# Kernel optimization log

Measured on AMD Instinct MI355X. Metric: run time of the kernel, lower is better.

The kernel has to match this reference:

```python
import jax, jax.numpy as jnp
import numpy as np
import math

S, H, NH, HD = 2048, 1280, 16, 80
WIN = 64
NW = S // WIN
I = 3420
OUT = 3584
L = 8
FULL_IDX = (3, 7)
MERGE = 4  # spatial_merge_size**2
EPS = 1e-6


def setup_inputs() -> dict:
    key = jax.random.key(0)
    ks = jax.random.split(key, 16)
    w = lambda k, s: jax.random.normal(k, s, jnp.float32) * 0.02
    # rotary tables: half-dim freqs duplicated, as in Qwen2.5-VL vision rotary
    inv_freq = 1.0 / (10000.0 ** (np.arange(0, HD // 2, dtype=np.float32) / (HD // 2)))
    freqs = np.outer(np.arange(S, dtype=np.float32), inv_freq)  # [S, HD/2]
    emb = np.concatenate([freqs, freqs], axis=-1)               # [S, HD]
    return {
        "hidden_states": jax.random.normal(ks[0], (S, H), jnp.float32),
        "full_attn_masks": jnp.ones((1, 1, S, S), jnp.float32),
        "window_attn_masks": jnp.ones((NW, 1, WIN, WIN), jnp.float32),
        "cos": jnp.asarray(np.cos(emb)),
        "sin": jnp.asarray(np.sin(emb)),
        "qkv_w": w(ks[1], (L, 3 * H, H)),
        "qkv_b": w(ks[2], (L, 3 * H)),
        "proj_w": w(ks[3], (L, H, H)),
        "proj_b": w(ks[4], (L, H)),
        "norm1_w": jnp.ones((L, H), jnp.float32),
        "norm2_w": jnp.ones((L, H), jnp.float32),
        "gate_w": w(ks[5], (L, I, H)),
        "gate_b": w(ks[6], (L, I)),
        "up_w": w(ks[7], (L, I, H)),
        "up_b": w(ks[8], (L, I)),
        "down_w": w(ks[9], (L, H, I)),
        "down_b": w(ks[10], (L, H)),
        "ln_q_w": jnp.ones((H,), jnp.float32),
        "m0_w": w(ks[11], (H * MERGE, H * MERGE)),
        "m0_b": w(ks[12], (H * MERGE,)),
        "m2_w": w(ks[13], (OUT, H * MERGE)),
        "m2_b": w(ks[14], (OUT,)),
    }


def rmsnorm(x, w):
    v = jnp.mean(jnp.square(x.astype(jnp.float32)), axis=-1, keepdims=True)
    return (x * jax.lax.rsqrt(v + EPS)) * w


def rotate_half(x):
    x1, x2 = jnp.split(x, 2, axis=-1)
    return jnp.concatenate([-x2, x1], axis=-1)


def apply_rope(q, k, cos, sin):
    return q * cos + rotate_half(q) * sin, k * cos + rotate_half(k) * sin


def attn_full(x, mask, cos, sin, qkv_w, qkv_b, proj_w, proj_b):
    # x: [S, H]; mask: [1, 1, S, S] (additive)
    qkv = (x @ qkv_w.T + qkv_b).reshape(S, 3, NH, HD)
    q, k, v = [t[:, i].transpose(1, 0, 2) for i, t in [(0, qkv), (1, qkv), (2, qkv)]]  # [NH, S, HD]
    q, k = apply_rope(q, k, cos, sin)  # cos/sin [S, HD] broadcast over heads
    aw = jnp.einsum('hsd,htd->hst', q, k) / math.sqrt(HD) + mask[0]
    aw = jax.nn.softmax(aw.astype(jnp.float32), axis=-1)
    o = jnp.einsum('hst,htd->hsd', aw, v).transpose(1, 0, 2).reshape(S, NH * HD)
    return o @ proj_w.T + proj_b


def attn_window(x, mask, cos, sin, qkv_w, qkv_b, proj_w, proj_b):
    xw = x.reshape(NW, WIN, H)
    qkv = (xw @ qkv_w.T + qkv_b).reshape(NW, WIN, 3, NH, HD).transpose(2, 0, 3, 1, 4)
    q, k, v = qkv[0], qkv[1], qkv[2]
    cw = cos.reshape(NW, 1, WIN, HD)
    sw = sin.reshape(NW, 1, WIN, HD)
    q, k = apply_rope(q, k, cw, sw)
    aw = jnp.einsum('whsd,whtd->whst', q, k) / math.sqrt(HD) + mask
    aw = jax.nn.softmax(aw.astype(jnp.float32), axis=-1)
    o = jnp.einsum('whst,whtd->whsd', aw, v).transpose(0, 2, 1, 3).reshape(S, NH * HD)
    return o @ proj_w.T + proj_b


def reference(hidden_states, full_attn_masks, window_attn_masks, cos, sin,
              qkv_w, qkv_b, proj_w, proj_b, norm1_w, norm2_w,
              gate_w, gate_b, up_w, up_b, down_w, down_b,
              ln_q_w, m0_w, m0_b, m2_w, m2_b):
    NEG = jnp.finfo(jnp.float32).min
    fm = (1.0 - full_attn_masks) * NEG
    wm = (1.0 - window_attn_masks) * NEG
    x = hidden_states
    for i in range(L):
        h = rmsnorm(x, norm1_w[i])
        if i in FULL_IDX:
            a = attn_full(h, fm, cos, sin, qkv_w[i], qkv_b[i], proj_w[i], proj_b[i])
        else:
            a = attn_window(h, wm, cos, sin, qkv_w[i], qkv_b[i], proj_w[i], proj_b[i])
        x = x + a
        h = rmsnorm(x, norm2_w[i])
        mlp = (jax.nn.silu(h @ gate_w[i].T + gate_b[i]) * (h @ up_w[i].T + up_b[i])) @ down_w[i].T + down_b[i]
        x = x + mlp
    # patch merger: RMSNorm -> merge 4 tokens -> Linear-GELU-Linear
    h = rmsnorm(x, ln_q_w).reshape(-1, H * MERGE)  # [S/4, 5120]
    h = jax.nn.gelu(h @ m0_w.T + m0_b, approximate=False)
    return h @ m2_w.T + m2_b  # [S/4, OUT]
```

## Files before the change

### kernel.cpp

```cpp
#include <hip/hip_runtime.h>
#include <hip/hip_bf16.h>
#include <math.h>

#define S_LEN 2048
#define HID   1280
#define NHEADS 16
#define HDIM  80
#define HDP   96
#define VROWS 96
#define LAYERS 8
#define IDIM  3420
#define IDIMP 3456
#define MERGED 5120
#define OUTD  3584
#define NCH   4
#define CHLEN 512

typedef __attribute__((ext_vector_type(8))) short short8;
typedef __attribute__((ext_vector_type(4))) float f32x4;
typedef __attribute__((ext_vector_type(16))) float f32x16;
typedef unsigned int u32;
typedef __attribute__((ext_vector_type(4))) u32 u32x4;
typedef __attribute__((address_space(1))) const u32* gptr_t;
typedef __attribute__((address_space(3))) u32* lptr_t;

__device__ inline unsigned short f2b(float f){
  __hip_bfloat16 b = __float2bfloat16(f);
  return __builtin_bit_cast(unsigned short, b);
}
__device__ inline float b2f(unsigned short u){
  return __bfloat162float(__builtin_bit_cast(__hip_bfloat16, u));
}
__device__ inline unsigned pk2(float lo, float hi){
  return (unsigned)f2b(lo) | ((unsigned)f2b(hi) << 16);
}

__global__ __launch_bounds__(256) void convert_kernel(
    const float* __restrict__ src, unsigned short* __restrict__ dst,
    int N, int K, int Np, int Kp)
{
  int kg = Kp >> 3;
  size_t total = (size_t)Np * kg;
  for (size_t i = (size_t)blockIdx.x * 256 + threadIdx.x; i < total;
       i += (size_t)gridDim.x * 256){
    int k8 = (int)(i % kg);
    int n  = (int)(i / kg);
    int k0 = k8 * 8;
    u32 out[4];
    if (n < N && k0 + 8 <= K){
      const float* s = src + (size_t)n * K + k0;
      float4 f0 = *(const float4*)s;
      float4 f1 = *(const float4*)(s + 4);
      out[0] = pk2(f0.x, f0.y); out[1] = pk2(f0.z, f0.w);
      out[2] = pk2(f1.x, f1.y); out[3] = pk2(f1.z, f1.w);
    } else {
      #pragma unroll
      for (int j = 0; j < 4; ++j){
        int ka = k0 + 2 * j;
        float lo = (n < N && ka     < K) ? src[(size_t)n * K + ka]     : 0.f;
        float hi = (n < N && ka + 1 < K) ? src[(size_t)n * K + ka + 1] : 0.f;
        out[j] = pk2(lo, hi);
      }
    }
    *(uint4*)(dst + i * 8) = make_uint4(out[0], out[1], out[2], out[3]);
  }
}

__global__ __launch_bounds__(256) void concat_bias_kernel(
    const float* __restrict__ g, const float* __restrict__ u, float* __restrict__ o)
{
  int n = blockIdx.x * 256 + threadIdx.x;
  if (n >= 2 * IDIMP) return;
  if (n < IDIMP) o[n] = (n < IDIM) ? g[n] : 0.f;
  else { int m2 = n - IDIMP; o[n] = (m2 < IDIM) ? u[m2] : 0.f; }
}

__global__ __launch_bounds__(256) void rmsnorm_kernel(
    const float* __restrict__ x, const float* __restrict__ w,
    unsigned short* __restrict__ out, int H)
{
  int s = blockIdx.x;
  const float* row = x + (size_t)s * H;
  float ss = 0.f;
  for (int c = threadIdx.x; c < H; c += 256){ float v = row[c]; ss += v * v; }
  #pragma unroll
  for (int off = 32; off >= 1; off >>= 1) ss += __shfl_xor(ss, off, 64);
  __shared__ float red[4];
  if ((threadIdx.x & 63) == 0) red[threadIdx.x >> 6] = ss;
  __syncthreads();
  ss = red[0] + red[1] + red[2] + red[3];
  float rs = rsqrtf(ss / H + 1e-6f);
  unsigned short* orow = out + (size_t)s * H;
  for (int c = threadIdx.x; c < H; c += 256) orow[c] = f2b(row[c] * rs * w[c]);
}

template<int EPI, int BM>
__global__ __launch_bounds__(256) void gemm_kernel(
    const unsigned short* __restrict__ A, int lda,
    const unsigned short* __restrict__ B, int ldb,
    const float* __restrict__ bias, int Nact,
    void* __restrict__ Cv, int ldc,
    const float* __restrict__ res,
    int K)
{
  constexpr int MI = BM / 32;
  __shared__ __align__(16) unsigned short As[2][BM * 32];
  __shared__ __align__(16) unsigned short Bs[2][4096];
  const int tid  = threadIdx.x;
  const int lane = tid & 63;
  const int wave = tid >> 6;
  const int wm = wave >> 1, wn = wave & 1;
  const int m0 = blockIdx.y * BM, n0 = blockIdx.x * 128;
  const int l16 = lane & 15, lh = lane >> 4;
  const int lrow = lane >> 2;
  const int lcol = lane & 3;
  f32x4 acc[MI][4] = {};

  auto stage = [&](int bufi, int k0){
    #pragma unroll
    for (int j = 0; j < BM / 64; ++j){
      int chunk = wave * (BM / 64) + j;
      int row  = chunk * 16 + lrow;
      int slot = lcol ^ ((row >> 1) & 3);
      const unsigned short* srcA = A + (size_t)(m0 + row) * lda + k0 + slot * 8;
      __builtin_amdgcn_global_load_lds((gptr_t)srcA, (lptr_t)&As[bufi][chunk * 512], 16, 0, 0);
    }
    #pragma unroll
    for (int j = 0; j < 2; ++j){
      int chunk = wave * 2 + j;
      int row  = chunk * 16 + lrow;
      int slot = lcol ^ ((row >> 1) & 3);
      const unsigned short* srcB = B + (size_t)(n0 + row) * ldb + k0 + slot * 8;
      __builtin_amdgcn_global_load_lds((gptr_t)srcB, (lptr_t)&Bs[bufi][chunk * 512], 16, 0, 0);
    }
  };

  const int nt = K >> 5;
  stage(0, 0);
  __syncthreads();
  int buf = 0;
  for (int t = 0; t < nt; ++t){
    if (t + 1 < nt) stage(buf ^ 1, (t + 1) << 5);
    short8 af[MI], bfr[4];
    #pragma unroll
    for (int mi = 0; mi < MI; ++mi){
      int r = wm * (BM / 2) + mi * 16 + l16;
      int sl = lh ^ ((r >> 1) & 3);
      af[mi] = *(const short8*)&As[buf][r * 32 + sl * 8];
    }
    #pragma unroll
    for (int ni = 0; ni < 4; ++ni){
      int r = wn * 64 + ni * 16 + l16;
      int sl = lh ^ ((r >> 1) & 3);
      bfr[ni] = *(const short8*)&Bs[buf][r * 32 + sl * 8];
    }
    #pragma unroll
    for (int mi = 0; mi < MI; ++mi)
      #pragma unroll
      for (int ni = 0; ni < 4; ++ni)
        acc[mi][ni] = __builtin_amdgcn_mfma_f32_16x16x32_bf16(af[mi], bfr[ni], acc[mi][ni], 0, 0, 0);
    __syncthreads();
    buf ^= 1;
  }

  #pragma unroll
  for (int mi = 0; mi < MI; ++mi){
    int row = m0 + wm * (BM / 2) + mi * 16 + lh * 4;
    #pragma unroll
    for (int ni = 0; ni < 4; ++ni){
      int gn = n0 + wn * 64 + ni * 16 + l16;
      float bv = (gn < Nact) ? bias[gn] : 0.f;
      #pragma unroll
      for (int r2 = 0; r2 < 4; ++r2){
        float v = acc[mi][ni][r2] + bv;
        size_t offc = (size_t)(row + r2) * ldc + gn;
        if (EPI == 0)      ((float*)Cv)[offc] = v;
        else if (EPI == 1) ((float*)Cv)[offc] = res[offc] + v;
        else if (EPI == 2) ((unsigned short*)Cv)[offc] = f2b(0.5f * v * (1.0f + erff(v * 0.70710678118f)));
        else               ((unsigned short*)Cv)[offc] = f2b(v);
      }
    }
  }
}

__global__ __launch_bounds__(256) void rope_split_kernel(
    const unsigned short* __restrict__ qkv, const float* __restrict__ cosT,
    const float* __restrict__ sinT,
    unsigned short* __restrict__ qo, unsigned short* __restrict__ ko,
    unsigned short* __restrict__ vt)
{
  int s = blockIdx.x;
  const unsigned short* row = qkv + (size_t)s * 3840;
  #pragma unroll
  for (int it = 0; it < 5; ++it){
    int idx = it * 256 + threadIdx.x;
    int h = idx / 80, d = idx % 80;
    float qv = b2f(row[h * 80 + d]);
    float kv = b2f(row[1280 + h * 80 + d]);
    float vv = b2f(row[2560 + h * 80 + d]);
    float c  = cosT[s * 80 + d], sn = sinT[s * 80 + d];
    float qr = (d < 40) ? -b2f(row[h * 80 + d + 40])        : b2f(row[h * 80 + d - 40]);
    float kr = (d < 40) ? -b2f(row[1280 + h * 80 + d + 40]) : b2f(row[1280 + h * 80 + d - 40]);
    size_t qkoff = ((size_t)h * S_LEN + s) * HDP + d;
    qo[qkoff] = f2b(qv * c + qr * sn);
    ko[qkoff] = f2b(kv * c + kr * sn);
    vt[((size_t)h * VROWS + d) * S_LEN + s] = f2b(vv);
  }
  int h2 = threadIdx.x >> 4, d2 = 80 + (threadIdx.x & 15);
  size_t poff = ((size_t)h2 * S_LEN + s) * HDP + d2;
  qo[poff] = 0; ko[poff] = 0;
}

template<int PART>
__global__ __launch_bounds__(256) void flash_kernel(
    const unsigned short* __restrict__ q, const unsigned short* __restrict__ k,
    const unsigned short* __restrict__ vt, unsigned short* __restrict__ out,
    float* __restrict__ opart, float* __restrict__ mlpart)
{
  __shared__ unsigned short ot[4][32][88];
  const int lane = threadIdx.x & 63;
  const int w = threadIdx.x >> 6;
  const int h = blockIdx.y;
  const int l31 = lane & 31, lh1 = lane >> 5;
  const int qr = blockIdx.x * 128 + w * 32;
  const int ch = PART ? blockIdx.z : 0;
  const unsigned short* qh = q + (size_t)h * S_LEN * HDP;
  const unsigned short* kh = k + (size_t)h * S_LEN * HDP;
  const unsigned short* vh = vt + (size_t)h * VROWS * S_LEN;

  short8 qa[5];
  #pragma unroll
  for (int kc = 0; kc < 5; ++kc)
    qa[kc] = *(const short8*)(qh + (size_t)(qr + l31) * HDP + kc * 16 + lh1 * 8);

  float m_ = -1e30f, l_ = 0.f;
  f32x16 o0 = {}, o1 = {}, o2 = {};
  const int kvb = PART ? ch * CHLEN : (qr & ~63);
  const int kve = PART ? ch * CHLEN + CHLEN : (qr & ~63) + 64;
  const float scale = 0.11180339887498949f;

  for (int kvt = kvb; kvt < kve; kvt += 32){
    f32x16 sc = {};
    __builtin_amdgcn_s_setprio(1);
    #pragma unroll
    for (int kc = 0; kc < 5; ++kc){
      short8 kf = *(const short8*)(kh + (size_t)(kvt + l31) * HDP + kc * 16 + lh1 * 8);
      sc = __builtin_amdgcn_mfma_f32_32x32x16_bf16(kf, qa[kc], sc, 0, 0, 0);
    }
    __builtin_amdgcn_s_setprio(0);
    float t = sc[0];
    #pragma unroll
    for (int i = 1; i < 16; ++i) t = fmaxf(t, sc[i]);
    t = fmaxf(t, __shfl_xor(t, 32)) * scale;
    if (!__all(t <= m_ + 8.f)){
      float mnew = fmaxf(m_, t);
      float corr = __expf(m_ - mnew);
      l_ *= corr;
      #pragma unroll
      for (int i = 0; i < 16; ++i){ o0[i] *= corr; o1[i] *= corr; o2[i] *= corr; }
      m_ = mnew;
    }
    float p[16];
    float rs = 0.f;
    #pragma unroll
    for (int i = 0; i < 16; ++i){ p[i] = __expf(sc[i] * scale - m_); rs += p[i]; }
    rs += __shfl_xor(rs, 32);
    l_ += rs;
    unsigned wd0[4], wd1[4];
    #pragma unroll
    for (int j = 0; j < 2; ++j){
      unsigned Aj = pk2(p[2 * j],     p[2 * j + 1]);
      unsigned Bj = pk2(p[4 + 2 * j], p[4 + 2 * j + 1]);
      unsigned t0 = __shfl_xor(Aj, 32);
      unsigned t1 = __shfl_xor(Bj, 32);
      wd0[j]     = lh1 ? t1 : Aj;
      wd0[2 + j] = lh1 ? Bj : t0;
      Aj = pk2(p[8 + 2 * j],  p[8 + 2 * j + 1]);
      Bj = pk2(p[12 + 2 * j], p[12 + 2 * j + 1]);
      t0 = __shfl_xor(Aj, 32);
      t1 = __shfl_xor(Bj, 32);
      wd1[j]     = lh1 ? t1 : Aj;
      wd1[2 + j] = lh1 ? Bj : t0;
    }
    __builtin_amdgcn_s_setprio(1);
    #pragma unroll
    for (int kc2 = 0; kc2 < 2; ++kc2){
      u32x4 uw = kc2 ? u32x4{wd1[0], wd1[1], wd1[2], wd1[3]}
                     : u32x4{wd0[0], wd0[1], wd0[2], wd0[3]};
      short8 pb = __builtin_bit_cast(short8, uw);
      const unsigned short* vb = vh + kvt + kc2 * 16 + lh1 * 8;
      o0 = __builtin_amdgcn_mfma_f32_32x32x16_bf16(
          *(const short8*)(vb + (size_t)(l31)      * S_LEN), pb, o0, 0, 0, 0);
      o1 = __builtin_amdgcn_mfma_f32_32x32x16_bf16(
          *(const short8*)(vb + (size_t)(32 + l31) * S_LEN), pb, o1, 0, 0, 0);
      o2 = __builtin_amdgcn_mfma_f32_32x32x16_bf16(
          *(const short8*)(vb + (size_t)(64 + l31) * S_LEN), pb, o2, 0, 0, 0);
    }
    __builtin_amdgcn_s_setprio(0);
  }

  if (PART){
    const size_t hb = (size_t)(ch * NHEADS + h) * 80;
    #pragma unroll
    for (int r = 0; r < 16; ++r){
      int dl = (r & 3) + 8 * (r >> 2) + 4 * lh1;
      opart[(hb + dl)      * S_LEN + qr + l31] = o0[r];
      opart[(hb + 32 + dl) * S_LEN + qr + l31] = o1[r];
      if (dl < 16) opart[(hb + 64 + dl) * S_LEN + qr + l31] = o2[r];
    }
    if (lane < 32){
      size_t mb = ((size_t)(ch * NHEADS + h) * S_LEN + qr + l31) * 2;
      mlpart[mb] = m_; mlpart[mb + 1] = l_;
    }
  } else {
    float inv = 1.f / l_;
    #pragma unroll
    for (int r = 0; r < 16; ++r){
      int dl = (r & 3) + 8 * (r >> 2) + 4 * lh1;
      ot[w][l31][dl]      = f2b(o0[r] * inv);
      ot[w][l31][32 + dl] = f2b(o1[r] * inv);
      if (dl < 16) ot[w][l31][64 + dl] = f2b(o2[r] * inv);
    }
    int qq = lane >> 1, half = lane & 1;
    #pragma unroll
    for (int j = 0; j < 20; ++j){
      unsigned v = *(const unsigned*)&ot[w][qq][half * 40 + j * 2];
      *(unsigned*)&out[(size_t)(qr + qq) * HID + h * HDIM + half * 40 + j * 2] = v;
    }
  }
}

__global__ __launch_bounds__(256) void flash_reduce_kernel(
    const float* __restrict__ opart, const float* __restrict__ mlpart,
    unsigned short* __restrict__ out)
{
  __shared__ float wn[NCH][256];
  __shared__ unsigned short ot[256][82];
  const int tid = threadIdx.x;
  const int h = blockIdx.y;
  const int q0 = blockIdx.x * 256;
  float mv[NCH], lv[NCH];
  float M = -1e30f;
  #pragma unroll
  for (int c = 0; c < NCH; ++c){
    size_t mb = ((size_t)(c * NHEADS + h) * S_LEN + q0 + tid) * 2;
    mv[c] = mlpart[mb]; lv[c] = mlpart[mb + 1];
    M = fmaxf(M, mv[c]);
  }
  float L = 0.f;
  #pragma unroll
  for (int c = 0; c < NCH; ++c){ mv[c] = __expf(mv[c] - M); L += mv[c] * lv[c]; }
  float invL = 1.f / L;
  #pragma unroll
  for (int c = 0; c < NCH; ++c) wn[c][tid] = mv[c] * invL;
  __syncthreads();
  for (int d = 0; d < HDIM; ++d){
    float acc = 0.f;
    #pragma unroll
    for (int c = 0; c < NCH; ++c)
      acc += wn[c][tid] * opart[((size_t)(c * NHEADS + h) * 80 + d) * S_LEN + q0 + tid];
    ot[tid][d] = f2b(acc);
  }
  __syncthreads();
  #pragma unroll
  for (int j = 0; j < 40; ++j){
    unsigned v = *(const unsigned*)&ot[tid][j * 2];
    *(unsigned*)&out[(size_t)(q0 + tid) * HID + h * HDIM + j * 2] = v;
  }
}

__global__ __launch_bounds__(256) void silu_mul_kernel(
    const float* __restrict__ gu, unsigned short* __restrict__ out)
{
  size_t i = ((size_t)blockIdx.x * 256 + threadIdx.x) * 4;
  if (i >= (size_t)S_LEN * IDIMP) return;
  int row = (int)(i / IDIMP), col = (int)(i % IDIMP);
  float4 gv = *(const float4*)(gu + (size_t)row * (2 * IDIMP) + col);
  float4 uv = *(const float4*)(gu + (size_t)row * (2 * IDIMP) + IDIMP + col);
  float r0 = gv.x / (1.f + __expf(-gv.x)) * uv.x;
  float r1 = gv.y / (1.f + __expf(-gv.y)) * uv.y;
  float r2 = gv.z / (1.f + __expf(-gv.z)) * uv.z;
  float r3 = gv.w / (1.f + __expf(-gv.w)) * uv.w;
  uint2 o;
  o.x = pk2(r0, r1); o.y = pk2(r2, r3);
  *(uint2*)(out + i) = o;
}

static inline int cgrid(size_t total){
  size_t b = (total + 255) / 256;
  return (int)(b < 4096 ? b : 4096);
}

extern "C" void kernel_launch(void* const* d_in, const int* in_sizes, int n_in,
                              void* d_out, int out_size, void* d_ws, size_t ws_size,
                              hipStream_t stream)
{
  const float* hidden = (const float*)d_in[0];
  const float* cosT   = (const float*)d_in[3];
  const float* sinT   = (const float*)d_in[4];
  const float* qkv_w  = (const float*)d_in[5];
  const float* qkv_b  = (const float*)d_in[6];
  const float* proj_w = (const float*)d_in[7];
  const float* proj_b = (const float*)d_in[8];
  const float* norm1_w= (const float*)d_in[9];
  const float* norm2_w= (const float*)d_in[10];
  const float* gate_w = (const float*)d_in[11];
  const float* gate_b = (const float*)d_in[12];
  const float* up_w   = (const float*)d_in[13];
  const float* up_b   = (const float*)d_in[14];
  const float* down_w = (const float*)d_in[15];
  const float* down_b = (const float*)d_in[16];
  const float* ln_q_w = (const float*)d_in[17];
  const float* m0_w   = (const float*)d_in[18];
  const float* m0_b   = (const float*)d_in[19];
  const float* m2_w   = (const float*)d_in[20];
  const float* m2_b   = (const float*)d_in[21];

  char* ws = (char*)d_ws;
  size_t off = 0;
  auto carve = [&](size_t bytes)->char*{
    char* p = ws + off; off += (bytes + 255) & ~(size_t)255; return p;
  };
  float*          x    = (float*)         carve((size_t)S_LEN * HID * 4);
  unsigned short* hbuf = (unsigned short*)carve((size_t)S_LEN * HID * 2);
  unsigned short* qkvb = (unsigned short*)carve((size_t)S_LEN * 3840 * 2);
  unsigned short* qp   = (unsigned short*)carve((size_t)NHEADS * S_LEN * HDP * 2);
  unsigned short* kp   = (unsigned short*)carve((size_t)NHEADS * S_LEN * HDP * 2);
  unsigned short* vtb  = (unsigned short*)carve((size_t)NHEADS * VROWS * S_LEN * 2);
  unsigned short* ao   = (unsigned short*)carve((size_t)S_LEN * HID * 2);
  float*          gbuf = (float*)         carve((size_t)S_LEN * 2 * IDIMP * 4);
  unsigned short* mlp  = (unsigned short*)carve((size_t)S_LEN * IDIMP * 2);
  unsigned short* mg   = (unsigned short*)carve((size_t)512 * MERGED * 2);
  float*          opart= (float*)         carve((size_t)NCH * NHEADS * 80 * S_LEN * 4);
  float*          mlpt = (float*)         carve((size_t)NCH * NHEADS * S_LEN * 2 * 4);
  float*          cbias= (float*)         carve((size_t)2 * IDIMP * 4);
  unsigned short* wbig = (unsigned short*)carve((size_t)45000000 * 2);
  unsigned short* wqkv = wbig;
  unsigned short* wproj= wbig +  4915200;
  unsigned short* wgate= wproj + 1638400;
  unsigned short* wup  = wgate + (size_t)IDIMP * HID;
  unsigned short* wdown= wup   + (size_t)IDIMP * HID;
  unsigned short* wm0  = wbig;
  unsigned short* wm2  = wbig + (size_t)MERGED * MERGED;
  (void)ws_size; (void)in_sizes; (void)n_in; (void)out_size;

  hipMemcpyAsync(x, hidden, (size_t)S_LEN * HID * 4, hipMemcpyDeviceToDevice, stream);

  for (int i = 0; i < LAYERS; ++i){
    convert_kernel<<<cgrid((size_t)3840*HID/8), 256, 0, stream>>>(
        qkv_w + (size_t)i*3840*HID, wqkv, 3840, HID, 3840, HID);
    convert_kernel<<<cgrid((size_t)HID*HID/8), 256, 0, stream>>>(
        proj_w + (size_t)i*HID*HID, wproj, HID, HID, HID, HID);
    convert_kernel<<<cgrid((size_t)IDIMP*HID/8), 256, 0, stream>>>(
        gate_w + (size_t)i*IDIM*HID, wgate, IDIM, HID, IDIMP, HID);
    convert_kernel<<<cgrid((size_t)IDIMP*HID/8), 256, 0, stream>>>(
        up_w + (size_t)i*IDIM*HID, wup, IDIM, HID, IDIMP, HID);
    convert_kernel<<<cgrid((size_t)HID*IDIMP/8), 256, 0, stream>>>(
        down_w + (size_t)i*HID*IDIM, wdown, HID, IDIM, HID, IDIMP);
    concat_bias_kernel<<<27, 256, 0, stream>>>(
        gate_b + (size_t)i*IDIM, up_b + (size_t)i*IDIM, cbias);

    rmsnorm_kernel<<<S_LEN, 256, 0, stream>>>(x, norm1_w + (size_t)i * HID, hbuf, HID);
    gemm_kernel<3,128><<<dim3(30, 16), 256, 0, stream>>>(
        hbuf, HID, wqkv, HID, qkv_b + (size_t)i * 3840, 3840,
        qkvb, 3840, nullptr, HID);
    rope_split_kernel<<<S_LEN, 256, 0, stream>>>(qkvb, cosT, sinT, qp, kp, vtb);
    if (i == 3 || i == 7){
      flash_kernel<1><<<dim3(16, 16, NCH), 256, 0, stream>>>(qp, kp, vtb, nullptr, opart, mlpt);
      flash_reduce_kernel<<<dim3(8, 16), 256, 0, stream>>>(opart, mlpt, ao);
    } else {
      flash_kernel<0><<<dim3(16, 16), 256, 0, stream>>>(qp, kp, vtb, ao, nullptr, nullptr);
    }
    gemm_kernel<1,64><<<dim3(10, 32), 256, 0, stream>>>(
        ao, HID, wproj, HID, proj_b + (size_t)i * HID, HID,
        x, HID, x, HID);
    rmsnorm_kernel<<<S_LEN, 256, 0, stream>>>(x, norm2_w + (size_t)i * HID, hbuf, HID);
    gemm_kernel<0,128><<<dim3(54, 16), 256, 0, stream>>>(
        hbuf, HID, wgate, HID, cbias, 2 * IDIMP,
        gbuf, 2 * IDIMP, nullptr, HID);
    silu_mul_kernel<<<(int)(((size_t)S_LEN * IDIMP / 4 + 255) / 256), 256, 0, stream>>>(gbuf, mlp);
    gemm_kernel<1,64><<<dim3(10, 32), 256, 0, stream>>>(
        mlp, IDIMP, wdown, IDIMP, down_b + (size_t)i * HID, HID,
        x, HID, x, IDIMP);
  }
  convert_kernel<<<cgrid((size_t)MERGED*MERGED/8), 256, 0, stream>>>(
      m0_w, wm0, MERGED, MERGED, MERGED, MERGED);
  convert_kernel<<<cgrid((size_t)OUTD*MERGED/8), 256, 0, stream>>>(
      m2_w, wm2, OUTD, MERGED, OUTD, MERGED);
  rmsnorm_kernel<<<S_LEN, 256, 0, stream>>>(x, ln_q_w, hbuf, HID);
  gemm_kernel<2,64><<<dim3(40, 8), 256, 0, stream>>>(
      hbuf, MERGED, wm0, MERGED, m0_b, MERGED, mg, MERGED, nullptr, MERGED);
  gemm_kernel<0,64><<<dim3(28, 8), 256, 0, stream>>>(
      mg, MERGED, wm2, MERGED, m2_b, OUTD, d_out, OUTD, nullptr, MERGED);
}
```

Measured before the change: 2.610 ms.

## Batch all weight conversions, vectorize rope split, store gate/up in bf16, more flash chunks

All 42 per-layer and merger weight fp32->bf16 conversions now run in one launch, using a segment table with a binary search per element, and biases are concatenated for all layers up front. This removes many small launches and tail effects. The rope/split kernel is reorganized per head and 128-row tile, with vectorized loads and an LDS-staged transpose for V, to coalesce the V^T writes. The gate/up GEMM now writes bf16 instead of fp32, halving that intermediate's traffic, and silu_mul reads 8 bf16 values per thread. The full-attention split-K chunk count doubles to 8, at the cost of more partial-reduction work and a little extra rounding.

New measurement: 2.753 ms. 5.5% more time.

```diff
diff --git a/kernel.cpp b/kernel.cpp
--- a/kernel.cpp
+++ b/kernel.cpp
@@ -13,8 +13,9 @@
 #define IDIMP 3456
 #define MERGED 5120
 #define OUTD  3584
-#define NCH   4
-#define CHLEN 512
+#define NCH   8
+#define CHLEN 256
+#define LWE   19824640LL
 
 typedef __attribute__((ext_vector_type(8))) short short8;
 typedef __attribute__((ext_vector_type(4))) float f32x4;
@@ -35,17 +36,43 @@
   return (unsigned)f2b(lo) | ((unsigned)f2b(hi) << 16);
 }
 
-__global__ __launch_bounds__(256) void convert_kernel(
-    const float* __restrict__ src, unsigned short* __restrict__ dst,
-    int N, int K, int Np, int Kp)
-{
-  int kg = Kp >> 3;
-  size_t total = (size_t)Np * kg;
+#define NSEG 42
+struct ConvSegs {
+  unsigned long long gpre[NSEG + 1];
+  long long srcoff[NSEG];
+  long long dstoff[NSEG];
+  int srcbase[NSEG];
+  int N[NSEG], K[NSEG], Np[NSEG], Kp[NSEG];
+};
+
+__global__ __launch_bounds__(256) void convert_all_kernel(
+    ConvSegs cs,
+    const float* __restrict__ b0, const float* __restrict__ b1,
+    const float* __restrict__ b2, const float* __restrict__ b3,
+    const float* __restrict__ b4, const float* __restrict__ b5,
+    const float* __restrict__ b6,
+    unsigned short* __restrict__ dst)
+{
+  size_t total = cs.gpre[NSEG];
   for (size_t i = (size_t)blockIdx.x * 256 + threadIdx.x; i < total;
        i += (size_t)gridDim.x * 256){
-    int k8 = (int)(i % kg);
-    int n  = (int)(i / kg);
+    int lo = 0, hi = NSEG - 1;
+    while (lo < hi){ int mid = (lo + hi + 1) >> 1;
+      if (cs.gpre[mid] <= i) lo = mid; else hi = mid - 1; }
+    size_t g = i - cs.gpre[lo];
+    int Kp = cs.Kp[lo], K = cs.K[lo], N = cs.N[lo];
+    int kg = Kp >> 3;
+    int k8 = (int)(g % kg);
+    int n  = (int)(g / kg);
     int k0 = k8 * 8;
+    const float* base;
+    switch (cs.srcbase[lo]){
+      case 0: base = b0; break; case 1: base = b1; break;
+      case 2: base = b2; break; case 3: base = b3; break;
+      case 4: base = b4; break; case 5: base = b5; break;
+      default: base = b6; break;
+    }
+    const float* src = base + cs.srcoff[lo];
     u32 out[4];
     if (n < N && k0 + 8 <= K){
       const float* s = src + (size_t)n * K + k0;
@@ -57,22 +84,26 @@
       #pragma unroll
       for (int j = 0; j < 4; ++j){
         int ka = k0 + 2 * j;
-        float lo = (n < N && ka     < K) ? src[(size_t)n * K + ka]     : 0.f;
-        float hi = (n < N && ka + 1 < K) ? src[(size_t)n * K + ka + 1] : 0.f;
-        out[j] = pk2(lo, hi);
+        float lv = (n < N && ka     < K) ? src[(size_t)n * K + ka]     : 0.f;
+        float hv = (n < N && ka + 1 < K) ? src[(size_t)n * K + ka + 1] : 0.f;
+        out[j] = pk2(lv, hv);
       }
     }
-    *(uint4*)(dst + i * 8) = make_uint4(out[0], out[1], out[2], out[3]);
+    *(uint4*)(dst + cs.dstoff[lo] + g * 8) = make_uint4(out[0], out[1], out[2], out[3]);
   }
 }
 
 __global__ __launch_bounds__(256) void concat_bias_kernel(
     const float* __restrict__ g, const float* __restrict__ u, float* __restrict__ o)
 {
+  int L = blockIdx.y;
   int n = blockIdx.x * 256 + threadIdx.x;
   if (n >= 2 * IDIMP) return;
-  if (n < IDIMP) o[n] = (n < IDIM) ? g[n] : 0.f;
-  else { int m2 = n - IDIMP; o[n] = (m2 < IDIM) ? u[m2] : 0.f; }
+  float* ol = o + (size_t)L * 2 * IDIMP;
+  const float* gl = g + (size_t)L * IDIM;
+  const float* ul = u + (size_t)L * IDIM;
+  if (n < IDIMP) ol[n] = (n < IDIM) ? gl[n] : 0.f;
+  else { int m2 = n - IDIMP; ol[n] = (m2 < IDIM) ? ul[m2] : 0.f; }
 }
 
 __global__ __launch_bounds__(256) void rmsnorm_kernel(
@@ -189,26 +220,60 @@
     unsigned short* __restrict__ qo, unsigned short* __restrict__ ko,
     unsigned short* __restrict__ vt)
 {
-  int s = blockIdx.x;
-  const unsigned short* row = qkv + (size_t)s * 3840;
+  __shared__ unsigned short vtile[80][128];
+  const int h = blockIdx.x;
+  const int s0 = blockIdx.y * 128;
+  const int t = threadIdx.x;
+  const int sr = t >> 1, half = t & 1;
+  const int s = s0 + sr;
+  const unsigned short* row = qkv + (size_t)s * 3840 + h * 80;
+  const float* crow = cosT + (size_t)s * 80;
+  const float* srow = sinT + (size_t)s * 80;
+  const float sgn = half ? 1.f : -1.f;
+  #pragma unroll
+  for (int g = 0; g < 5; ++g){
+    int d  = half * 40 + g * 8;
+    int dp = 40 - half * 40 + g * 8;
+    short8 q8  = *(const short8*)(row + d);
+    short8 k8  = *(const short8*)(row + 1280 + d);
+    short8 qp8 = *(const short8*)(row + dp);
+    short8 kp8 = *(const short8*)(row + 1280 + dp);
+    short8 v8  = *(const short8*)(row + 2560 + d);
+    float4 c0  = *(const float4*)(crow + d);
+    float4 c1  = *(const float4*)(crow + d + 4);
+    float4 sn0 = *(const float4*)(srow + d);
+    float4 sn1 = *(const float4*)(srow + d + 4);
+    float cc[8] = {c0.x, c0.y, c0.z, c0.w, c1.x, c1.y, c1.z, c1.w};
+    float ss[8] = {sn0.x, sn0.y, sn0.z, sn0.w, sn1.x, sn1.y, sn1.z, sn1.w};
+    short8 qo8, ko8;
+    #pragma unroll
+    for (int j = 0; j < 8; ++j){
+      float qv = b2f((unsigned short)q8[j]);
+      float kv = b2f((unsigned short)k8[j]);
+      float qr = sgn * b2f((unsigned short)qp8[j]);
+      float kr = sgn * b2f((unsigned short)kp8[j]);
+      qo8[j] = (short)f2b(qv * cc[j] + qr * ss[j]);
+      ko8[j] = (short)f2b(kv * cc[j] + kr * ss[j]);
+      vtile[d + j][sr] = (unsigned short)v8[j];
+    }
+    size_t qkoff = ((size_t)h * S_LEN + s) * HDP + d;
+    *(short8*)(qo + qkoff) = qo8;
+    *(short8*)(ko + qkoff) = ko8;
+  }
+  {
+    short8 z = {};
+    size_t poff = ((size_t)h * S_LEN + s) * HDP + 80 + half * 8;
+    *(short8*)(qo + poff) = z;
+    *(short8*)(ko + poff) = z;
+  }
+  __syncthreads();
   #pragma unroll
   for (int it = 0; it < 5; ++it){
-    int idx = it * 256 + threadIdx.x;
-    int h = idx / 80, d = idx % 80;
-    float qv = b2f(row[h * 80 + d]);
-    float kv = b2f(row[1280 + h * 80 + d]);
-    float vv = b2f(row[2560 + h * 80 + d]);
-    float c  = cosT[s * 80 + d], sn = sinT[s * 80 + d];
-    float qr = (d < 40) ? -b2f(row[h * 80 + d + 40])        : b2f(row[h * 80 + d - 40]);
-    float kr = (d < 40) ? -b2f(row[1280 + h * 80 + d + 40]) : b2f(row[1280 + h * 80 + d - 40]);
-    size_t qkoff = ((size_t)h * S_LEN + s) * HDP + d;
-    qo[qkoff] = f2b(qv * c + qr * sn);
-    ko[qkoff] = f2b(kv * c + kr * sn);
-    vt[((size_t)h * VROWS + d) * S_LEN + s] = f2b(vv);
-  }
-  int h2 = threadIdx.x >> 4, d2 = 80 + (threadIdx.x & 15);
-  size_t poff = ((size_t)h2 * S_LEN + s) * HDP + d2;
-  qo[poff] = 0; ko[poff] = 0;
+    int j = t + it * 256;
+    int d = j >> 4, ch = j & 15;
+    uint4 v = *(const uint4*)&vtile[d][ch * 8];
+    *(uint4*)(vt + ((size_t)h * VROWS + d) * S_LEN + s0 + ch * 8) = v;
+  }
 }
 
 template<int PART>
@@ -370,25 +435,21 @@
 }
 
 __global__ __launch_bounds__(256) void silu_mul_kernel(
-    const float* __restrict__ gu, unsigned short* __restrict__ out)
-{
-  size_t i = ((size_t)blockIdx.x * 256 + threadIdx.x) * 4;
+    const unsigned short* __restrict__ gu, unsigned short* __restrict__ out)
+{
+  size_t i = ((size_t)blockIdx.x * 256 + threadIdx.x) * 8;
   if (i >= (size_t)S_LEN * IDIMP) return;
   int row = (int)(i / IDIMP), col = (int)(i % IDIMP);
-  float4 gv = *(const float4*)(gu + (size_t)row * (2 * IDIMP) + col);
-  float4 uv = *(const float4*)(gu + (size_t)row * (2 * IDIMP) + IDIMP + col);
-  float r0 = gv.x / (1.f + __expf(-gv.x)) * uv.x;
-  float r1 = gv.y / (1.f + __expf(-gv.y)) * uv.y;
-  float r2 = gv.z / (1.f + __expf(-gv.z)) * uv.z;
-  float r3 = gv.w / (1.f + __expf(-gv.w)) * uv.w;
-  uint2 o;
-  o.x = pk2(r0, r1); o.y = pk2(r2, r3);
-  *(uint2*)(out + i) = o;
-}
-
-static inline int cgrid(size_t total){
-  size_t b = (total + 255) / 256;
-  return (int)(b < 4096 ? b : 4096);
+  short8 g8 = *(const short8*)(gu + (size_t)row * (2 * IDIMP) + col);
+  short8 u8 = *(const short8*)(gu + (size_t)row * (2 * IDIMP) + IDIMP + col);
+  short8 o8;
+  #pragma unroll
+  for (int j = 0; j < 8; ++j){
+    float gv = b2f((unsigned short)g8[j]);
+    float uv = b2f((unsigned short)u8[j]);
+    o8[j] = (short)f2b(gv / (1.f + __expf(-gv)) * uv);
+  }
+  *(short8*)(out + i) = o8;
 }
 
 extern "C" void kernel_launch(void* const* d_in, const int* in_sizes, int n_in,
@@ -428,43 +489,52 @@
   unsigned short* kp   = (unsigned short*)carve((size_t)NHEADS * S_LEN * HDP * 2);
   unsigned short* vtb  = (unsigned short*)carve((size_t)NHEADS * VROWS * S_LEN * 2);
   unsigned short* ao   = (unsigned short*)carve((size_t)S_LEN * HID * 2);
-  float*          gbuf = (float*)         carve((size_t)S_LEN * 2 * IDIMP * 4);
+  unsigned short* gbuf = (unsigned short*)carve((size_t)S_LEN * 2 * IDIMP * 2);
   unsigned short* mlp  = (unsigned short*)carve((size_t)S_LEN * IDIMP * 2);
   unsigned short* mg   = (unsigned short*)carve((size_t)512 * MERGED * 2);
   float*          opart= (float*)         carve((size_t)NCH * NHEADS * 80 * S_LEN * 4);
   float*          mlpt = (float*)         carve((size_t)NCH * NHEADS * S_LEN * 2 * 4);
-  float*          cbias= (float*)         carve((size_t)2 * IDIMP * 4);
-  unsigned short* wbig = (unsigned short*)carve((size_t)45000000 * 2);
-  unsigned short* wqkv = wbig;
-  unsigned short* wproj= wbig +  4915200;
-  unsigned short* wgate= wproj + 1638400;
-  unsigned short* wup  = wgate + (size_t)IDIMP * HID;
-  unsigned short* wdown= wup   + (size_t)IDIMP * HID;
-  unsigned short* wm0  = wbig;
-  unsigned short* wm2  = wbig + (size_t)MERGED * MERGED;
+  float*          cbias= (float*)         carve((size_t)LAYERS * 2 * IDIMP * 4);
+  unsigned short* wbf  = (unsigned short*)carve((size_t)203161600 * 2);
   (void)ws_size; (void)in_sizes; (void)n_in; (void)out_size;
 
+  ConvSegs cs;
+  {
+    unsigned long long g = 0; int si = 0;
+    auto add = [&](int base, long long soff, long long doff, int N, int K, int Np, int Kp){
+      cs.gpre[si] = g; cs.srcbase[si] = base; cs.srcoff[si] = soff; cs.dstoff[si] = doff;
+      cs.N[si] = N; cs.K[si] = K; cs.Np[si] = Np; cs.Kp[si] = Kp;
+      g += (unsigned long long)Np * (Kp >> 3); ++si;
+    };
+    for (long long i = 0; i < LAYERS; ++i){
+      add(0, i * 3840LL * HID, i * LWE + 0,        3840, HID, 3840, HID);
+      add(1, i * (long long)HID * HID, i * LWE + 4915200,  HID, HID, HID, HID);
+      add(2, i * (long long)IDIM * HID, i * LWE + 6553600,  IDIM, HID, IDIMP, HID);
+      add(3, i * (long long)IDIM * HID, i * LWE + 10977280, IDIM, HID, IDIMP, HID);
+      add(4, i * (long long)HID * IDIM, i * LWE + 15400960, HID, IDIM, HID, IDIMP);
+    }
+    add(5, 0, 8 * LWE,            MERGED, MERGED, MERGED, MERGED);
+    add(6, 0, 8 * LWE + 26214400, OUTD,   MERGED, OUTD,   MERGED);
+    cs.gpre[NSEG] = g;
+  }
+
+  convert_all_kernel<<<4096, 256, 0, stream>>>(
+      cs, qkv_w, proj_w, gate_w, up_w, down_w, m0_w, m2_w, wbf);
+  concat_bias_kernel<<<dim3(27, LAYERS), 256, 0, stream>>>(gate_b, up_b, cbias);
   hipMemcpyAsync(x, hidden, (size_t)S_LEN * HID * 4, hipMemcpyDeviceToDevice, stream);
 
   for (int i = 0; i < LAYERS; ++i){
-    convert_kernel<<<cgrid((size_t)3840*HID/8), 256, 0, stream>>>(
-        qkv_w + (size_t)i*3840*HID, wqkv, 3840, HID, 3840, HID);
-    convert_kernel<<<cgrid((size_t)HID*HID/8), 256, 0, stream>>>(
-        proj_w + (size_t)i*HID*HID, wproj, HID, HID, HID, HID);
-    convert_kernel<<<cgrid((size_t)IDIMP*HID/8), 256, 0, stream>>>(
-        gate_w + (size_t)i*IDIM*HID, wgate, IDIM, HID, IDIMP, HID);
-    convert_kernel<<<cgrid((size_t)IDIMP*HID/8), 256, 0, stream>>>(
-        up_w + (size_t)i*IDIM*HID, wup, IDIM, HID, IDIMP, HID);
-    convert_kernel<<<cgrid((size_t)HID*IDIMP/8), 256, 0, stream>>>(
-        down_w + (size_t)i*HID*IDIM, wdown, HID, IDIM, HID, IDIMP);
-    concat_bias_kernel<<<27, 256, 0, stream>>>(
-        gate_b + (size_t)i*IDIM, up_b + (size_t)i*IDIM, cbias);
+    unsigned short* wl = wbf + (size_t)i * LWE;
+    unsigned short* wqkv = wl;
+    unsigned short* wproj= wl + 4915200;
+    unsigned short* wgate= wl + 6553600;
+    unsigned short* wdown= wl + 15400960;
 
     rmsnorm_kernel<<<S_LEN, 256, 0, stream>>>(x, norm1_w + (size_t)i * HID, hbuf, HID);
     gemm_kernel<3,128><<<dim3(30, 16), 256, 0, stream>>>(
         hbuf, HID, wqkv, HID, qkv_b + (size_t)i * 3840, 3840,
         qkvb, 3840, nullptr, HID);
-    rope_split_kernel<<<S_LEN, 256, 0, stream>>>(qkvb, cosT, sinT, qp, kp, vtb);
+    rope_split_kernel<<<dim3(NHEADS, 16), 256, 0, stream>>>(qkvb, cosT, sinT, qp, kp, vtb);
     if (i == 3 || i == 7){
       flash_kernel<1><<<dim3(16, 16, NCH), 256, 0, stream>>>(qp, kp, vtb, nullptr, opart, mlpt);
       flash_reduce_kernel<<<dim3(8, 16), 256, 0, stream>>>(opart, mlpt, ao);
@@ -475,18 +545,16 @@
         ao, HID, wproj, HID, proj_b + (size_t)i * HID, HID,
         x, HID, x, HID);
     rmsnorm_kernel<<<S_LEN, 256, 0, stream>>>(x, norm2_w + (size_t)i * HID, hbuf, HID);
-    gemm_kernel<0,128><<<dim3(54, 16), 256, 0, stream>>>(
-        hbuf, HID, wgate, HID, cbias, 2 * IDIMP,
+    gemm_kernel<3,128><<<dim3(54, 16), 256, 0, stream>>>(
+        hbuf, HID, wgate, HID, cbias + (size_t)i * 2 * IDIMP, 2 * IDIMP,
         gbuf, 2 * IDIMP, nullptr, HID);
-    silu_mul_kernel<<<(int)(((size_t)S_LEN * IDIMP / 4 + 255) / 256), 256, 0, stream>>>(gbuf, mlp);
+    silu_mul_kernel<<<(int)(((size_t)S_LEN * IDIMP / 8 + 255) / 256), 256, 0, stream>>>(gbuf, mlp);
     gemm_kernel<1,64><<<dim3(10, 32), 256, 0, stream>>>(
         mlp, IDIMP, wdown, IDIMP, down_b + (size_t)i * HID, HID,
         x, HID, x, IDIMP);
   }
-  convert_kernel<<<cgrid((size_t)MERGED*MERGED/8), 256, 0, stream>>>(
-      m0_w, wm0, MERGED, MERGED, MERGED, MERGED);
-  convert_kernel<<<cgrid((size_t)OUTD*MERGED/8), 256, 0, stream>>>(
-      m2_w, wm2, OUTD, MERGED, OUTD, MERGED);
+  unsigned short* wm0 = wbf + 8 * LWE;
+  unsigned short* wm2 = wm0 + (size_t)MERGED * MERGED;
   rmsnorm_kernel<<<S_LEN, 256, 0, stream>>>(x, ln_q_w, hbuf, HID);
   gemm_kernel<2,64><<<dim3(40, 8), 256, 0, stream>>>(
       hbuf, MERGED, wm0, MERGED, m0_b, MERGED, mg, MERGED, nullptr, MERGED);
```
